# Kernel optimization log

Hardware: AMD Instinct MI355X
Metric: run time of the kernel (lower is better)

## Reference

```python
import jax, jax.numpy as jnp
import numpy as np

NUM_NODES = 100000
NUM_EDGES = 100000  # matches edge_idx.max()+1 with randint(0, NUM_EDGES)
K = 16
NNZ = 3200000
EPS = 1e-6
LAMBDA_SEP = 0.1


def setup_inputs() -> dict:
    key = jax.random.key(0)
    k1, k2 = jax.random.split(key)
    Z = jax.random.normal(k1, (NUM_NODES, K), dtype=jnp.float32)
    hyperedge_index = jax.random.randint(k2, (2, NNZ), 0, NUM_EDGES, dtype=jnp.int64)
    return {"Z": Z, "hyperedge_index": hyperedge_index, "num_nodes": NUM_NODES}


def reference(Z, hyperedge_index, num_nodes):
    node_idx = hyperedge_index[0]
    edge_idx = hyperedge_index[1]

    # Degree vectors Dv, De via scatter-add of ones
    ones_pin = jnp.ones(node_idx.shape, dtype=Z.dtype)
    Dv = jax.ops.segment_sum(ones_pin, node_idx, num_segments=num_nodes)
    De = jax.ops.segment_sum(ones_pin, edge_idx, num_segments=NUM_EDGES)
    Dv = jnp.clip(Dv, EPS, None)
    De = jnp.clip(De, EPS, None)

    Dv_inv_sqrt = Dv ** -0.5  # [N]
    nZ = Dv_inv_sqrt[:, None] * Z  # [N, k], normalized embeddings

    # Per-hyperedge sums of normalized embeddings, all k columns at once
    # (vectorizes the torch per-k loop; same math)
    S = jax.ops.segment_sum(nZ[node_idx], edge_idx, num_segments=NUM_EDGES)  # [E, k]

    # theta_j = sum_e w(e)/De(e) * S[e,j]^2 with w(e)=1
    theta = jnp.sum(S * S / De[:, None], axis=0)  # [k]

    # f^T Dv f per column, clamped
    f_Dv_f = jnp.clip(jnp.sum(Z * Z * Dv[:, None], axis=0), EPS, None)  # [k]

    rq = 1.0 - theta / f_Dv_f
    rq = jnp.where(jnp.isfinite(rq), rq, 0.0)
    rayleigh_loss = jnp.mean(rq)

    # Fiedler separation penalty on column 0
    f = Z[:, 0]
    pos = f > 0
    neg = f < 0
    pos_cnt = jnp.sum(pos)
    neg_cnt = jnp.sum(neg)
    pos_mean = jnp.sum(jnp.where(pos, f, 0.0)) / jnp.maximum(pos_cnt, 1).astype(f.dtype)
    neg_mean = jnp.sum(jnp.where(neg, f, 0.0)) / jnp.maximum(neg_cnt, 1).astype(f.dtype)
    separation = jnp.abs(pos_mean - neg_mean)
    sep_penalty = jnp.where((pos_cnt == 0) | (neg_cnt == 0), 1.0, 1.0 / (separation + EPS))

    # contrastive loss is 0 (no hint_partition / cut_size_func); kl is 0 (no mu/logvar)
    return rayleigh_loss + LAMBDA_SEP * sep_penalty
```

## Files before the change

### kernel.cpp

```cpp
#include <hip/hip_runtime.h>
#include <hip/hip_fp16.h>
#include <math.h>
#include <stdint.h>

#define NNZ_C 3200000
#define NN_C  100000
#define NE_C  100000
#define KD    16
#define EPSF  1e-6f
#define LSEP  0.1f

typedef unsigned int uint_t;

#define W_PK    0
#define W_ACC   50000
#define W_S     50064
#define W_NZ    (W_S + NE_C * KD)
#define W_END   (W_NZ + NN_C * KD / 2)
#define W_ZERO  W_NZ

__device__ __forceinline__ void lds_fadd(float* p, float v) {
    asm volatile("ds_add_f32 %0, %1"
                 :
                 : "v"((uint32_t)(uintptr_t)p), "v"(v));
}

__device__ __forceinline__ float deg_from_packed(const uint_t* __restrict__ packed,
                                                 int base_word, int idx) {
    uint_t w = packed[base_word + (idx >> 2)];
    return (float)((w >> ((idx & 3) * 8)) & 255u);
}

__global__ __launch_bounds__(512) void k_hist(const int* __restrict__ il,
                                              uint_t* __restrict__ packed) {
    __shared__ uint_t h[12500];
    int t = threadIdx.x, b = blockIdx.x;
    int hist  = b >> 7;
    int range = (b >> 6) & 1;
    int slice = b & 63;

    for (int w = t; w < 12500; w += 512) h[w] = 0u;
    __syncthreads();

    const int4* idx4 = (const int4*)(il + (size_t)hist * NNZ_C + (size_t)slice * 50000);
    uint_t base = (uint_t)range * 50000u;
    for (int i = t; i < 12500; i += 512) {
        int4 v = idx4[i];
        uint_t u;
        u = (uint_t)v.x - base; if (u < 50000u) atomicAdd(&h[u >> 2], 1u << ((u & 3u) * 8u));
        u = (uint_t)v.y - base; if (u < 50000u) atomicAdd(&h[u >> 2], 1u << ((u & 3u) * 8u));
        u = (uint_t)v.z - base; if (u < 50000u) atomicAdd(&h[u >> 2], 1u << ((u & 3u) * 8u));
        u = (uint_t)v.w - base; if (u < 50000u) atomicAdd(&h[u >> 2], 1u << ((u & 3u) * 8u));
    }
    __syncthreads();

    uint_t* gp = packed + hist * 25000 + range * 12500;
    for (int w = t; w < 12500; w += 512) {
        uint_t v = h[w];
        if (v) atomicAdd(&gp[w], v);
    }
}

__global__ __launch_bounds__(256) void k_norm(const float* __restrict__ Z,
                                              const uint_t* __restrict__ packed,
                                              __half* __restrict__ nZh,
                                              float* __restrict__ acc) {
    __shared__ float sacc[KD + 4];
    int t = threadIdx.x;
    if (t < KD + 4) sacc[t] = 0.f;
    __syncthreads();

    int n = blockIdx.x * 256 + t;
    if (n < NN_C) {
        float dv = fmaxf(deg_from_packed(packed, 0, n), EPSF);
        float inv = rsqrtf(dv);
        const float4* z4 = (const float4*)(Z + (size_t)n * KD);
        float zr[KD];
        #pragma unroll
        for (int i = 0; i < 4; ++i) {
            float4 z = z4[i];
            zr[4*i+0] = z.x; zr[4*i+1] = z.y; zr[4*i+2] = z.z; zr[4*i+3] = z.w;
        }
        uint4 u[2];
        __half2* hu = (__half2*)u;
        #pragma unroll
        for (int j = 0; j < 8; ++j)
            hu[j] = __floats2half2_rn(zr[2*j] * inv, zr[2*j+1] * inv);
        uint4* o = (uint4*)(nZh + (size_t)n * KD);
        o[0] = u[0];
        o[1] = u[1];
        #pragma unroll
        for (int k = 0; k < KD; ++k) lds_fadd(&sacc[k], zr[k] * zr[k] * dv);
        float f = zr[0];
        if (f > 0.f)      { lds_fadd(&sacc[KD+0], f); lds_fadd(&sacc[KD+2], 1.f); }
        else if (f < 0.f) { lds_fadd(&sacc[KD+1], f); lds_fadd(&sacc[KD+3], 1.f); }
    }
    __syncthreads();
    if (t < KD)          unsafeAtomicAdd(&acc[16 + t], sacc[t]);
    else if (t < KD + 4) unsafeAtomicAdd(&acc[32 + (t - KD)], sacc[t]);
}

__global__ __launch_bounds__(256) void k_scatter(const int* __restrict__ il,
                                                 const __half* __restrict__ nZh,
                                                 float* __restrict__ S) {
    uint_t tid = blockIdx.x * 256u + threadIdx.x;
    if (tid < (uint_t)NNZ_C * KD) {
        uint_t p = tid >> 4, k = tid & 15u;
        int n = il[p];
        int e = il[NNZ_C + p];
        float v = __half2float(nZh[(size_t)n * KD + k]);
        unsafeAtomicAdd(&S[(size_t)e * KD + k], v);
    }
}

__global__ __launch_bounds__(256) void k_theta(const float* __restrict__ S,
                                               const uint_t* __restrict__ packed,
                                               float* __restrict__ acc) {
    __shared__ float sacc[KD];
    int t = threadIdx.x;
    if (t < KD) sacc[t] = 0.f;
    __syncthreads();
    int e = blockIdx.x * 256 + t;
    if (e < NE_C) {
        float rinv = 1.f / fmaxf(deg_from_packed(packed, 25000, e), EPSF);
        const float4* s4 = (const float4*)(S + (size_t)e * KD);
        #pragma unroll
        for (int i = 0; i < 4; ++i) {
            float4 s = s4[i];
            lds_fadd(&sacc[4*i+0], s.x * s.x * rinv);
            lds_fadd(&sacc[4*i+1], s.y * s.y * rinv);
            lds_fadd(&sacc[4*i+2], s.z * s.z * rinv);
            lds_fadd(&sacc[4*i+3], s.w * s.w * rinv);
        }
    }
    __syncthreads();
    if (t < KD) unsafeAtomicAdd(&acc[t], sacc[t]);
}

__global__ void k_final(const float* __restrict__ acc, float* __restrict__ out) {
    if (blockIdx.x == 0 && threadIdx.x == 0) {
        float rsum = 0.f;
        #pragma unroll
        for (int k = 0; k < KD; ++k) {
            float theta = acc[k];
            float fd    = fmaxf(acc[16 + k], EPSF);
            float rq    = 1.f - theta / fd;
            if (!isfinite(rq)) rq = 0.f;
            rsum += rq;
        }
        float rl = rsum / (float)KD;
        float pS = acc[32], nS = acc[33], pC = acc[34], nC = acc[35];
        float pm = pS / fmaxf(pC, 1.f);
        float nm = nS / fmaxf(nC, 1.f);
        float sep = fabsf(pm - nm);
        float pen = (pC == 0.f || nC == 0.f) ? 1.f : 1.f / (sep + EPSF);
        out[0] = rl + LSEP * pen;
    }
}

extern "C" void kernel_launch(void* const* d_in, const int* in_sizes, int n_in,
                              void* d_out, int out_size, void* d_ws, size_t ws_size,
                              hipStream_t stream) {
    const float* Z  = (const float*)d_in[0];
    const int*   il = (const int*)d_in[1];
    float*  ws     = (float*)d_ws;
    uint_t* packed = (uint_t*)d_ws + W_PK;
    float*  acc    = ws + W_ACC;
    float*  S      = ws + W_S;
    __half* nZh    = (__half*)(ws + W_NZ);
    float*  out    = (float*)d_out;

    hipMemsetAsync(ws, 0, (size_t)W_ZERO * sizeof(float), stream);

    k_hist  <<<256, 512, 0, stream>>>(il, packed);
    k_norm  <<<(NN_C + 255) / 256, 256, 0, stream>>>(Z, packed, nZh, acc);
    {
        uint_t total = (uint_t)NNZ_C * KD;
        k_scatter<<<(total + 255) / 256, 256, 0, stream>>>(il, nZh, S);
    }
    k_theta <<<(NE_C + 255) / 256, 256, 0, stream>>>(S, packed, acc);
    k_final <<<1, 64, 0, stream>>>(acc, out);
}
```

Measured before the change: 232.4 us.

## Merge final reduction into theta kernel and use full-range LDS histograms

The separate k_final launch is removed. k_theta now uses a global atomic ticket so the last block reads the accumulators and writes the loss, which saves one kernel launch. k_hist now keeps the whole 100K-bin packed histogram in about 100KB of dynamic LDS with 128 blocks instead of 256 range-split blocks, so each index is read once rather than twice. The cost is lower occupancy from the large LDS footprint and a fence plus atomic counter at the end of k_theta.

After: 258.0 us. 1.11x slower.

```diff
diff --git a/kernel.cpp b/kernel.cpp
--- a/kernel.cpp
+++ b/kernel.cpp
@@ -19,6 +19,8 @@
 #define W_END   (W_NZ + NN_C * KD / 2)
 #define W_ZERO  W_NZ
 
+#define THETA_BLOCKS ((NE_C + 255) / 256)
+
 __device__ __forceinline__ void lds_fadd(float* p, float v) {
     asm volatile("ds_add_f32 %0, %1"
                  :
@@ -33,29 +35,27 @@
 
 __global__ __launch_bounds__(512) void k_hist(const int* __restrict__ il,
                                               uint_t* __restrict__ packed) {
-    __shared__ uint_t h[12500];
+    extern __shared__ uint_t h[];
     int t = threadIdx.x, b = blockIdx.x;
-    int hist  = b >> 7;
-    int range = (b >> 6) & 1;
+    int hist  = b >> 6;
     int slice = b & 63;
 
-    for (int w = t; w < 12500; w += 512) h[w] = 0u;
+    for (int w = t; w < 25000; w += 512) h[w] = 0u;
     __syncthreads();
 
     const int4* idx4 = (const int4*)(il + (size_t)hist * NNZ_C + (size_t)slice * 50000);
-    uint_t base = (uint_t)range * 50000u;
     for (int i = t; i < 12500; i += 512) {
         int4 v = idx4[i];
         uint_t u;
-        u = (uint_t)v.x - base; if (u < 50000u) atomicAdd(&h[u >> 2], 1u << ((u & 3u) * 8u));
-        u = (uint_t)v.y - base; if (u < 50000u) atomicAdd(&h[u >> 2], 1u << ((u & 3u) * 8u));
-        u = (uint_t)v.z - base; if (u < 50000u) atomicAdd(&h[u >> 2], 1u << ((u & 3u) * 8u));
-        u = (uint_t)v.w - base; if (u < 50000u) atomicAdd(&h[u >> 2], 1u << ((u & 3u) * 8u));
+        u = (uint_t)v.x; atomicAdd(&h[u >> 2], 1u << ((u & 3u) * 8u));
+        u = (uint_t)v.y; atomicAdd(&h[u >> 2], 1u << ((u & 3u) * 8u));
+        u = (uint_t)v.z; atomicAdd(&h[u >> 2], 1u << ((u & 3u) * 8u));
+        u = (uint_t)v.w; atomicAdd(&h[u >> 2], 1u << ((u & 3u) * 8u));
     }
     __syncthreads();
 
-    uint_t* gp = packed + hist * 25000 + range * 12500;
-    for (int w = t; w < 12500; w += 512) {
+    uint_t* gp = packed + hist * 25000;
+    for (int w = t; w < 25000; w += 512) {
         uint_t v = h[w];
         if (v) atomicAdd(&gp[w], v);
     }
@@ -115,8 +115,10 @@
 
 __global__ __launch_bounds__(256) void k_theta(const float* __restrict__ S,
                                                const uint_t* __restrict__ packed,
-                                               float* __restrict__ acc) {
+                                               float* __restrict__ acc,
+                                               float* __restrict__ out) {
     __shared__ float sacc[KD];
+    __shared__ uint_t lastflag;
     int t = threadIdx.x;
     if (t < KD) sacc[t] = 0.f;
     __syncthreads();
@@ -135,21 +137,28 @@
     }
     __syncthreads();
     if (t < KD) unsafeAtomicAdd(&acc[t], sacc[t]);
-}
 
-__global__ void k_final(const float* __restrict__ acc, float* __restrict__ out) {
-    if (blockIdx.x == 0 && threadIdx.x == 0) {
+    __threadfence();
+    if (t == 0) {
+        uint_t old = atomicAdd((uint_t*)(acc + 63), 1u);
+        lastflag = (old == (uint_t)(THETA_BLOCKS - 1));
+    }
+    __syncthreads();
+    if (lastflag && t == 0) {
+        float a[36];
+        #pragma unroll
+        for (int i = 0; i < 36; ++i) a[i] = unsafeAtomicAdd(&acc[i], 0.f);
         float rsum = 0.f;
         #pragma unroll
         for (int k = 0; k < KD; ++k) {
-            float theta = acc[k];
-            float fd    = fmaxf(acc[16 + k], EPSF);
+            float theta = a[k];
+            float fd    = fmaxf(a[16 + k], EPSF);
             float rq    = 1.f - theta / fd;
             if (!isfinite(rq)) rq = 0.f;
             rsum += rq;
         }
         float rl = rsum / (float)KD;
-        float pS = acc[32], nS = acc[33], pC = acc[34], nC = acc[35];
+        float pS = a[32], nS = a[33], pC = a[34], nC = a[35];
         float pm = pS / fmaxf(pC, 1.f);
         float nm = nS / fmaxf(nC, 1.f);
         float sep = fabsf(pm - nm);
@@ -172,12 +181,11 @@
 
     hipMemsetAsync(ws, 0, (size_t)W_ZERO * sizeof(float), stream);
 
-    k_hist  <<<256, 512, 0, stream>>>(il, packed);
-    k_norm  <<<(NN_C + 255) / 256, 256, 0, stream>>>(Z, packed, nZh, acc);
+    k_hist <<<128, 512, 100000, stream>>>(il, packed);
+    k_norm <<<(NN_C + 255) / 256, 256, 0, stream>>>(Z, packed, nZh, acc);
     {
         uint_t total = (uint_t)NNZ_C * KD;
         k_scatter<<<(total + 255) / 256, 256, 0, stream>>>(il, nZh, S);
     }
-    k_theta <<<(NE_C + 255) / 256, 256, 0, stream>>>(S, packed, acc);
-    k_final <<<1, 64, 0, stream>>>(acc, out);
+    k_theta<<<THETA_BLOCKS, 256, 0, stream>>>(S, packed, acc, out);
 }
```
